# Optimization experiments

Measured on AMD Instinct MI355X. Metric: run time of the kernel, lower is better.

## Reference

```python
import jax, jax.numpy as jnp
import numpy as np

L1, L2, N, C = 4096, 4096, 8, 3


def setup_inputs() -> dict:
    key = jax.random.key(0)
    k1, k2 = jax.random.split(key)
    coords1 = jax.random.uniform(k1, (L1, N, C), dtype=jnp.float32)
    coords2 = jax.random.uniform(k2, (L2, N, C), dtype=jnp.float32)
    return {"coords1": coords1, "coords2": coords2}


def reference(coords1, coords2):
    # coords1: [L1, N, C], coords2: [L2, N, C]
    l1, n, c = coords1.shape
    l2 = coords2.shape[0]
    # Batch-first layout, matching flatten_batch semantics (per-batch NN only)
    q = jnp.swapaxes(coords2, 0, 1)  # [N, L2, C] query points
    r = jnp.swapaxes(coords1, 0, 1)  # [N, L1, C] reference points
    # Squared euclidean distances per batch: [N, L2, L1]
    d2 = (
        jnp.sum(q * q, axis=-1)[:, :, None]
        + jnp.sum(r * r, axis=-1)[:, None, :]
        - 2.0 * jnp.einsum("nlc,nmc->nlm", q, r)
    )
    # tc.nearest returns global flat index; original does fmod(L1) to get the
    # per-batch index — argmin within each batch gives that directly.
    nearest = jnp.argmin(d2, axis=-1)  # [N, L2]
    clusters = nearest.T  # [L2, N]
    # torch.meshgrid(arange(L2), arange(N)) with 'ij' indexing; indices[-1] is
    # the batch index broadcast to [L2, N].
    batch_idx = jnp.broadcast_to(jnp.arange(n, dtype=jnp.int64 if False else jnp.int32), (l2, n))
    return (clusters.reshape(-1), batch_idx.reshape(-1))
```

## Files before the change

### kernel.cpp

```cpp
#include <hip/hip_runtime.h>
#include <float.h>


typedef float v2f __attribute__((ext_vector_type(2)));

constexpr int kL1 = 4096, kL2 = 4096, kN = 8;

__global__ __launch_bounds__(256, 2)
void nearest_kernel(const float* __restrict__ c1, const float* __restrict__ c2,
                    int* __restrict__ out) {
#pragma clang fp contract(off)
  __shared__ float4 refs[kL1];

  const int tid = threadIdx.x;
  const int n = blockIdx.y;

#pragma unroll
  for (int k = 0; k < kL1 / 256; ++k) {
    const int j = tid + 256 * k;
    const float* p = c1 + (j * kN + n) * 3;
    const float r0 = p[0], r1 = p[1], r2 = p[2];
    const float rr = __fadd_rn(
        __fadd_rn(__fmul_rn(r0, r0), __fmul_rn(r1, r1)), __fmul_rn(r2, r2));
    refs[j] = make_float4(r0, r1, r2, rr);
  }

  const int g = tid >> 3;
  const int lane8 = tid & 7;
  const int qa = blockIdx.x * 64 + g * 2;
  const int qb = qa + 1;

  const float* pa = c2 + (qa * kN + n) * 3;
  const float* pb = c2 + (qb * kN + n) * 3;
  const v2f qx = {pa[0], pb[0]};
  const v2f qy = {pa[1], pb[1]};
  const v2f qz = {pa[2], pb[2]};
  const v2f qq = {
      __fadd_rn(__fadd_rn(__fmul_rn(qx.x, qx.x), __fmul_rn(qy.x, qy.x)),
                __fmul_rn(qz.x, qz.x)),
      __fadd_rn(__fadd_rn(__fmul_rn(qx.y, qx.y), __fmul_rn(qy.y, qy.y)),
                __fmul_rn(qz.y, qz.y))};

  __syncthreads();

  v2f bd0 = {FLT_MAX, FLT_MAX}, bd1 = {FLT_MAX, FLT_MAX};
  int bi0a = 0, bi0b = 0, bi1a = 0, bi1b = 0;

#pragma unroll 2
  for (int t = 0; t < kL1 / 16; ++t) {
    const int j0 = lane8 + 16 * t;
    const float4 rA = refs[j0];
    const float4 rB = refs[j0 + 8];
    {
      const v2f m0 = qx * rA.x;
      const v2f m1 = qy * rA.y;
      const v2f s01 = m0 + m1;
      const v2f m2 = qz * rA.z;
      const v2f dot = s01 + m2;
      const v2f A = qq + rA.w;
      const float da = __fmaf_rn(-2.0f, dot.x, A.x);
      const float db = __fmaf_rn(-2.0f, dot.y, A.y);
      if (da < bd0.x) { bd0.x = da; bi0a = j0; }
      if (db < bd0.y) { bd0.y = db; bi0b = j0; }
    }
    {
      const v2f m0 = qx * rB.x;
      const v2f m1 = qy * rB.y;
      const v2f s01 = m0 + m1;
      const v2f m2 = qz * rB.z;
      const v2f dot = s01 + m2;
      const v2f A = qq + rB.w;
      const float da = __fmaf_rn(-2.0f, dot.x, A.x);
      const float db = __fmaf_rn(-2.0f, dot.y, A.y);
      if (da < bd1.x) { bd1.x = da; bi1a = j0 + 8; }
      if (db < bd1.y) { bd1.y = db; bi1b = j0 + 8; }
    }
  }

  float bda = bd0.x; int bia = bi0a;
  if (bd1.x < bda || (bd1.x == bda && bi1a < bia)) { bda = bd1.x; bia = bi1a; }
  float bdb = bd0.y; int bib = bi0b;
  if (bd1.y < bdb || (bd1.y == bdb && bi1b < bib)) { bdb = bd1.y; bib = bi1b; }

#pragma unroll
  for (int m = 1; m <= 4; m <<= 1) {
    const float oda = __shfl_xor(bda, m);
    const int oia = __shfl_xor(bia, m);
    if (oda < bda || (oda == bda && oia < bia)) { bda = oda; bia = oia; }
    const float odb = __shfl_xor(bdb, m);
    const int oib = __shfl_xor(bib, m);
    if (odb < bdb || (odb == bdb && oib < bib)) { bdb = odb; bib = oib; }
  }

  if (lane8 == 0) {
    out[qa * kN + n] = bia;
    out[qb * kN + n] = bib;
    out[kL2 * kN + qa * kN + n] = n;
    out[kL2 * kN + qb * kN + n] = n;
  }
}

extern "C" void kernel_launch(void* const* d_in, const int* in_sizes, int n_in,
                              void* d_out, int out_size, void* d_ws, size_t ws_size,
                              hipStream_t stream) {
  const float* c1 = (const float*)d_in[0];
  const float* c2 = (const float*)d_in[1];
  int* out = (int*)d_out;
  dim3 grid(kL2 / 64, kN);
  nearest_kernel<<<grid, dim3(256), 0, stream>>>(c1, c2, out);
}
```

Baseline: 92.38 us.

## Chunk reference points in LDS and split each query across 16 lanes

Result: faster. 89.34 us (-3.3%).

```diff
diff --git a/kernel.cpp b/kernel.cpp
--- a/kernel.cpp
+++ b/kernel.cpp
@@ -5,29 +5,21 @@
 typedef float v2f __attribute__((ext_vector_type(2)));
 
 constexpr int kL1 = 4096, kL2 = 4096, kN = 8;
+constexpr int kChunk = 2048;
+constexpr int kQPerBlock = 32;
 
-__global__ __launch_bounds__(256, 2)
+__global__ __launch_bounds__(256, 4)
 void nearest_kernel(const float* __restrict__ c1, const float* __restrict__ c2,
                     int* __restrict__ out) {
 #pragma clang fp contract(off)
-  __shared__ float4 refs[kL1];
+  __shared__ float4 refs[kChunk];
 
   const int tid = threadIdx.x;
   const int n = blockIdx.y;
 
-#pragma unroll
-  for (int k = 0; k < kL1 / 256; ++k) {
-    const int j = tid + 256 * k;
-    const float* p = c1 + (j * kN + n) * 3;
-    const float r0 = p[0], r1 = p[1], r2 = p[2];
-    const float rr = __fadd_rn(
-        __fadd_rn(__fmul_rn(r0, r0), __fmul_rn(r1, r1)), __fmul_rn(r2, r2));
-    refs[j] = make_float4(r0, r1, r2, rr);
-  }
-
-  const int g = tid >> 3;
-  const int lane8 = tid & 7;
-  const int qa = blockIdx.x * 64 + g * 2;
+  const int g = tid >> 4;
+  const int lane16 = tid & 15;
+  const int qa = blockIdx.x * kQPerBlock + g * 2;
   const int qb = qa + 1;
 
   const float* pa = c2 + (qa * kN + n) * 3;
@@ -41,39 +33,53 @@
       __fadd_rn(__fadd_rn(__fmul_rn(qx.y, qx.y), __fmul_rn(qy.y, qy.y)),
                 __fmul_rn(qz.y, qz.y))};
 
-  __syncthreads();
-
   v2f bd0 = {FLT_MAX, FLT_MAX}, bd1 = {FLT_MAX, FLT_MAX};
   int bi0a = 0, bi0b = 0, bi1a = 0, bi1b = 0;
 
+  for (int chunk = 0; chunk < kL1 / kChunk; ++chunk) {
+    __syncthreads();
+
+#pragma unroll
+    for (int k = 0; k < kChunk / 256; ++k) {
+      const int j = tid + 256 * k;
+      const float* p = c1 + ((chunk * kChunk + j) * kN + n) * 3;
+      const float r0 = p[0], r1 = p[1], r2 = p[2];
+      const float rr = __fadd_rn(
+          __fadd_rn(__fmul_rn(r0, r0), __fmul_rn(r1, r1)), __fmul_rn(r2, r2));
+      refs[j] = make_float4(r0, r1, r2, rr);
+    }
+    __syncthreads();
+
+    const int base = chunk * kChunk;
 #pragma unroll 2
-  for (int t = 0; t < kL1 / 16; ++t) {
-    const int j0 = lane8 + 16 * t;
-    const float4 rA = refs[j0];
-    const float4 rB = refs[j0 + 8];
-    {
-      const v2f m0 = qx * rA.x;
-      const v2f m1 = qy * rA.y;
-      const v2f s01 = m0 + m1;
-      const v2f m2 = qz * rA.z;
-      const v2f dot = s01 + m2;
-      const v2f A = qq + rA.w;
-      const float da = __fmaf_rn(-2.0f, dot.x, A.x);
-      const float db = __fmaf_rn(-2.0f, dot.y, A.y);
-      if (da < bd0.x) { bd0.x = da; bi0a = j0; }
-      if (db < bd0.y) { bd0.y = db; bi0b = j0; }
-    }
-    {
-      const v2f m0 = qx * rB.x;
-      const v2f m1 = qy * rB.y;
-      const v2f s01 = m0 + m1;
-      const v2f m2 = qz * rB.z;
-      const v2f dot = s01 + m2;
-      const v2f A = qq + rB.w;
-      const float da = __fmaf_rn(-2.0f, dot.x, A.x);
-      const float db = __fmaf_rn(-2.0f, dot.y, A.y);
-      if (da < bd1.x) { bd1.x = da; bi1a = j0 + 8; }
-      if (db < bd1.y) { bd1.y = db; bi1b = j0 + 8; }
+    for (int t = 0; t < kChunk / 32; ++t) {
+      const int j0 = lane16 + 32 * t;
+      const float4 rA = refs[j0];
+      const float4 rB = refs[j0 + 16];
+      {
+        const v2f m0 = qx * rA.x;
+        const v2f m1 = qy * rA.y;
+        const v2f s01 = m0 + m1;
+        const v2f m2 = qz * rA.z;
+        const v2f dot = s01 + m2;
+        const v2f A = qq + rA.w;
+        const float da = __fmaf_rn(-2.0f, dot.x, A.x);
+        const float db = __fmaf_rn(-2.0f, dot.y, A.y);
+        if (da < bd0.x) { bd0.x = da; bi0a = base + j0; }
+        if (db < bd0.y) { bd0.y = db; bi0b = base + j0; }
+      }
+      {
+        const v2f m0 = qx * rB.x;
+        const v2f m1 = qy * rB.y;
+        const v2f s01 = m0 + m1;
+        const v2f m2 = qz * rB.z;
+        const v2f dot = s01 + m2;
+        const v2f A = qq + rB.w;
+        const float da = __fmaf_rn(-2.0f, dot.x, A.x);
+        const float db = __fmaf_rn(-2.0f, dot.y, A.y);
+        if (da < bd1.x) { bd1.x = da; bi1a = base + j0 + 16; }
+        if (db < bd1.y) { bd1.y = db; bi1b = base + j0 + 16; }
+      }
     }
   }
 
@@ -83,7 +89,7 @@
   if (bd1.y < bdb || (bd1.y == bdb && bi1b < bib)) { bdb = bd1.y; bib = bi1b; }
 
 #pragma unroll
-  for (int m = 1; m <= 4; m <<= 1) {
+  for (int m = 1; m <= 8; m <<= 1) {
     const float oda = __shfl_xor(bda, m);
     const int oia = __shfl_xor(bia, m);
     if (oda < bda || (oda == bda && oia < bia)) { bda = oda; bia = oia; }
@@ -92,7 +98,7 @@
     if (odb < bdb || (odb == bdb && oib < bib)) { bdb = odb; bib = oib; }
   }
 
-  if (lane8 == 0) {
+  if (lane16 == 0) {
     out[qa * kN + n] = bia;
     out[qb * kN + n] = bib;
     out[kL2 * kN + qa * kN + n] = n;
@@ -106,6 +112,6 @@
   const float* c1 = (const float*)d_in[0];
   const float* c2 = (const float*)d_in[1];
   int* out = (int*)d_out;
-  dim3 grid(kL2 / 64, kN);
+  dim3 grid(kL2 / kQPerBlock, kN);
   nearest_kernel<<<grid, dim3(256), 0, stream>>>(c1, c2, out);
 }
```
